# Performance work log

Hardware: AMD Instinct MI355X
Metric: run time of the kernel (lower is better)

Reference implementation:

```python
import jax, jax.numpy as jnp
import numpy as np

NUM_HEADS = 12
HEAD_SIZE = 64
HIDDEN = NUM_HEADS * HEAD_SIZE  # 768
SEQ = 4096


def setup_inputs() -> dict:
    key = jax.random.key(0)
    ks = jax.random.split(key, 7)
    s = 0.02
    return {
        "hidden_states": jax.random.normal(ks[0], (1, SEQ, HIDDEN), jnp.float32),
        "attention_mask": jnp.zeros((1, 1, 1, SEQ), jnp.float32),
        "Wq": jax.random.normal(ks[1], (HIDDEN, HIDDEN), jnp.float32) * s,
        "bq": jax.random.normal(ks[2], (HIDDEN,), jnp.float32) * s,
        "Wk": jax.random.normal(ks[3], (HIDDEN, HIDDEN), jnp.float32) * s,
        "bk": jax.random.normal(ks[4], (HIDDEN,), jnp.float32) * s,
        "Wv": jax.random.normal(ks[5], (HIDDEN, HIDDEN), jnp.float32) * s,
        "bv": jax.random.normal(ks[6], (HIDDEN,), jnp.float32) * s,
    }


def _split_heads(x):
    # [B, S, H] -> [B, nh, S, hd]
    B, S, _ = x.shape
    return x.reshape(B, S, NUM_HEADS, HEAD_SIZE).transpose(0, 2, 1, 3)


def reference(hidden_states, attention_mask, Wq, bq, Wk, bk, Wv, bv):
    # torch Linear: y = x @ W.T + b
    q = _split_heads(hidden_states @ Wq.T + bq)  # [B, nh, S, hd]
    k = _split_heads(hidden_states @ Wk.T + bk)
    scores = jnp.einsum("bhqd,bhkd->bhqk", q, k) / jnp.sqrt(
        jnp.asarray(HEAD_SIZE, hidden_states.dtype)
    )
    scores = scores + attention_mask  # broadcast [1,1,1,S]
    probs = jax.nn.softmax(scores, axis=-1)  # [B, nh, S, S]
    # multi_rand_attn_cuda is a Monte-Carlo approximation of the exact
    # aggregation: probs @ (hidden @ Wv.T + bv), per head. The reference
    # computes the exact expected value (deterministic equivalent).
    v = _split_heads(hidden_states @ Wv.T + bv)  # [B, nh, S, hd]
    ctx = jnp.einsum("bhqk,bhkd->bhqd", probs, v)  # [B, nh, S, hd]
    B, _, S, _ = ctx.shape
    ctx = ctx.transpose(0, 2, 1, 3).reshape(B, S, HIDDEN)
    return ctx
```

## Files before the change

kernel.cpp:

```cpp
#include <hip/hip_runtime.h>
#include <hip/hip_bf16.h>

#define SEQ 4096
#define HID 768
#define NHEAD 12
#define HDIM 64
#define KVB 64
#define NT (SEQ / KVB)
#define PBK 64
#define PNT (HID / PBK)

typedef __attribute__((ext_vector_type(8))) short bf16x8;
typedef __attribute__((ext_vector_type(4))) float f32x4;
typedef __attribute__((ext_vector_type(4))) short s16x4;

static __device__ __forceinline__ short f2bf(float f) {
    unsigned u = __builtin_bit_cast(unsigned, f);
    unsigned r = (u + 0x7fffu + ((u >> 16) & 1u)) >> 16;
    return (short)r;
}
static __device__ __forceinline__ unsigned cvtpk(float lo, float hi) {
    unsigned r;
    asm("v_cvt_pk_bf16_f32 %0, %1, %2" : "=v"(r) : "v"(lo), "v"(hi));
    return r;
}
static __device__ __forceinline__ float max3f(float a, float b, float c) {
    float r;
    asm("v_max3_f32 %0, %1, %2, %3" : "=v"(r) : "v"(a), "v"(b), "v"(c));
    return r;
}
static __device__ __forceinline__ void glds16(const void* g, void* l) {
    __builtin_amdgcn_global_load_lds(
        (const __attribute__((address_space(1))) unsigned*)g,
        (__attribute__((address_space(3))) unsigned*)l, 16, 0, 0);
}

__global__ __launch_bounds__(256) void cast_bf16_kernel(
    const float* __restrict__ src, short* __restrict__ dst)
{
    const size_t i = (size_t)blockIdx.x * 256 + threadIdx.x;
    const float4* s = reinterpret_cast<const float4*>(src) + i * 2;
    const float4 a = s[0], b = s[1];
    bf16x8 o;
    o[0] = f2bf(a.x); o[1] = f2bf(a.y); o[2] = f2bf(a.z); o[3] = f2bf(a.w);
    o[4] = f2bf(b.x); o[5] = f2bf(b.y); o[6] = f2bf(b.z); o[7] = f2bf(b.w);
    reinterpret_cast<bf16x8*>(dst)[i] = o;
}

__global__ __launch_bounds__(256) void cast_w_kernel(
    const float* __restrict__ Wq, const float* __restrict__ Wk,
    const float* __restrict__ Wv, short* __restrict__ dst)
{
    const int z = blockIdx.y;
    const float* src = (z == 0) ? Wq : ((z == 1) ? Wk : Wv);
    const size_t i = (size_t)blockIdx.x * 256 + threadIdx.x;
    const float4* s = reinterpret_cast<const float4*>(src) + i * 2;
    const float4 a = s[0], b = s[1];
    bf16x8 o;
    o[0] = f2bf(a.x); o[1] = f2bf(a.y); o[2] = f2bf(a.z); o[3] = f2bf(a.w);
    o[4] = f2bf(b.x); o[5] = f2bf(b.y); o[6] = f2bf(b.z); o[7] = f2bf(b.w);
    reinterpret_cast<bf16x8*>(dst + (size_t)z * HID * HID)[i] = o;
}

__global__ __launch_bounds__(256) void qkv_proj_kernel(
    const short* __restrict__ hsb, const short* __restrict__ Wb,
    const float* __restrict__ bq, const float* __restrict__ bk,
    const float* __restrict__ bv,
    short* __restrict__ Qb, short* __restrict__ Kb, short* __restrict__ Vt)
{
    __shared__ __align__(16) char lds[65536];
    const int z = blockIdx.z;
    const float* bias = (z == 0) ? bq : ((z == 1) ? bk : bv);

    const int lane = threadIdx.x & 63;
    const int w    = threadIdx.x >> 6;
    const int lr = lane & 15, hi = lane >> 4;
    const int wi = w >> 1, wj = w & 1;

    const short* Ag; const short* Bg; int ar0, br0;
    if (z < 2) { Ag = Wb + (size_t)z * HID * HID; ar0 = blockIdx.x * 128;
                 Bg = hsb;                        br0 = blockIdx.y * 128; }
    else       { Ag = hsb;                        ar0 = blockIdx.y * 128;
                 Bg = Wb + (size_t)2 * HID * HID; br0 = blockIdx.x * 128; }

    const int rsub = lane >> 3;
    const int c16  = (lane & 7) ^ rsub;

    auto stage = [&](int t, int buf) {
        const int k0 = t * PBK;
#pragma unroll
        for (int c = 0; c < 4; ++c) {
            const int ch = w * 4 + c;
            const int row = ch * 8 + rsub;
            glds16(Ag + (size_t)(ar0 + row) * HID + k0 + c16 * 8,
                   lds + buf * 16384 + ch * 1024);
            glds16(Bg + (size_t)(br0 + row) * HID + k0 + c16 * 8,
                   lds + 32768 + buf * 16384 + ch * 1024);
        }
    };

    stage(0, 0);
    f32x4 acc[4][4] = {};

    for (int t = 0; t < PNT; ++t) {
        asm volatile("s_waitcnt vmcnt(0)" ::: "memory");
        __builtin_amdgcn_s_barrier();
        __builtin_amdgcn_sched_barrier(0);
        if (t + 1 < PNT) stage(t + 1, (t + 1) & 1);
        const char* LA = lds + (t & 1) * 16384;
        const char* LB = lds + 32768 + (t & 1) * 16384;
#pragma unroll
        for (int ks = 0; ks < 2; ++ks) {
            bf16x8 af[4], bf_[4];
#pragma unroll
            for (int i = 0; i < 4; ++i) {
                const int rowA = wi * 64 + i * 16 + lr;
                af[i] = *reinterpret_cast<const bf16x8*>(
                    LA + rowA * 128 + (((ks * 4 + hi) ^ (rowA & 7)) << 4));
                const int rowB = wj * 64 + i * 16 + lr;
                bf_[i] = *reinterpret_cast<const bf16x8*>(
                    LB + rowB * 128 + (((ks * 4 + hi) ^ (rowB & 7)) << 4));
            }
            __builtin_amdgcn_s_setprio(1);
#pragma unroll
            for (int ia = 0; ia < 4; ++ia)
#pragma unroll
                for (int ib = 0; ib < 4; ++ib)
                    acc[ia][ib] = __builtin_amdgcn_mfma_f32_16x16x32_bf16(
                        af[ia], bf_[ib], acc[ia][ib], 0, 0, 0);
            __builtin_amdgcn_s_setprio(0);
        }
    }

    const float SCQ = 0.125f * 1.44269504088896340736f;
    if (z < 2) {
        short* outp = (z == 0) ? Qb : Kb;
        const float sc = (z == 0) ? SCQ : 1.0f;
#pragma unroll
        for (int ia = 0; ia < 4; ++ia) {
            const int nb = ar0 + wi * 64 + ia * 16 + hi * 4;
            const float4 b4 = *reinterpret_cast<const float4*>(bias + nb);
#pragma unroll
            for (int ib = 0; ib < 4; ++ib) {
                const int m = br0 + wj * 64 + ib * 16 + lr;
                s16x4 v;
                v[0] = f2bf((acc[ia][ib][0] + b4.x) * sc);
                v[1] = f2bf((acc[ia][ib][1] + b4.y) * sc);
                v[2] = f2bf((acc[ia][ib][2] + b4.z) * sc);
                v[3] = f2bf((acc[ia][ib][3] + b4.w) * sc);
                *reinterpret_cast<s16x4*>(outp + (size_t)m * HID + nb) = v;
            }
        }
    } else {
#pragma unroll
        for (int ib = 0; ib < 4; ++ib) {
            const int n = br0 + wj * 64 + ib * 16 + lr;
            const float bb = bias[n];
#pragma unroll
            for (int ia = 0; ia < 4; ++ia) {
                const int mb = ar0 + wi * 64 + ia * 16 + hi * 4;
                s16x4 v;
                v[0] = f2bf(acc[ia][ib][0] + bb);
                v[1] = f2bf(acc[ia][ib][1] + bb);
                v[2] = f2bf(acc[ia][ib][2] + bb);
                v[3] = f2bf(acc[ia][ib][3] + bb);
                *reinterpret_cast<s16x4*>(Vt + (size_t)n * SEQ + mb) = v;
            }
        }
    }
}

__global__ __launch_bounds__(512, 6) void attn_kernel(
    const short* __restrict__ Qb, const short* __restrict__ Kb,
    const short* __restrict__ Vt, const float* __restrict__ maskp,
    float* __restrict__ out)
{
    __shared__ __align__(16) char lds[49152];
    const int tid  = threadIdx.x;
    const int lane = tid & 63;
    const int w    = tid >> 6;
    const int lr = lane & 15, hi = lane >> 4;
    const int qh = w >> 1, kh = w & 1;
    const int head = blockIdx.y;
    const int q0 = blockIdx.x * 64 + qh * 16;
    const float ML = 1.44269504088896340736f;

    const int srow = lane >> 3;
    const int c16s = (lane & 7) ^ srow ^ ((w & 1) << 2);
    const int sofK = (w * 8 + srow) * HID + head * HDIM + c16s * 8;
    const int sofV = (head * HDIM + w * 8 + srow) * SEQ + c16s * 8;
    const short* gK = Kb;
    const short* gV = Vt;
    char* sdK = lds + w * 1024;
    char* sdV = lds + 16384 + w * 1024;

    auto stagep = [&](int buf) {
        glds16(gK + sofK, sdK + buf * 8192);
        glds16(gV + sofV, sdV + buf * 8192);
        gK += KVB * HID; gV += KVB;
    };

    stagep(0);

    {
        float* mb = (float*)(lds + 32768);
        const int base = tid * 8;
#pragma unroll
        for (int i = 0; i < 2; ++i) {
            float4 m4 = *reinterpret_cast<const float4*>(maskp + base + i * 4);
            m4.x *= ML; m4.y *= ML; m4.z *= ML; m4.w *= ML;
            *reinterpret_cast<float4*>(mb + base + i * 4) = m4;
        }
    }

    const short* qp = Qb + (size_t)(q0 + lr) * HID + head * HDIM + hi * 8;
    const bf16x8 qf0 = *reinterpret_cast<const bf16x8*>(qp);
    const bf16x8 qf1 = *reinterpret_cast<const bf16x8*>(qp + 32);

    __syncthreads();

    const int kbase = ((lr >> 2) * 8) + (lr & 3);
    const int krow0 = kh * 32 + kbase;
    const int fr0   = (krow0 & 7) ^ (((krow0 >> 3) & 1) << 2);
    const int o1    = (hi ^ fr0) << 4;
    const char* kpA = lds + krow0 * 128 + o1;
    const char* kpB = lds + krow0 * 128 + (o1 ^ 64);
    const int fv    = (lr & 7) ^ (((lr >> 3) & 1) << 2);
    const char* vpB = lds + 16384 + lr * 128 + (((kh * 4 + hi) ^ fv) << 4);
    const float* mptr = (const float*)(lds + 32768) + kh * 32 + hi * 8;

    f32x4 acc[4] = {};
    float m_r = -INFINITY, ls = 0.f;

    auto tile = [&](int tt, int buf) {
        asm volatile("s_waitcnt vmcnt(0)" ::: "memory");
        __builtin_amdgcn_s_barrier();
        __builtin_amdgcn_sched_barrier(0);
        if (tt + 1 < NT) stagep(buf ^ 1);

        const f32x4 ci0 = *reinterpret_cast<const f32x4*>(mptr);
        const f32x4 ci1 = *reinterpret_cast<const f32x4*>(mptr + 4);
        mptr += KVB;
        const int bo = buf * 8192;
        const bf16x8 kf00 = *reinterpret_cast<const bf16x8*>(kpA + bo);
        const bf16x8 kf01 = *reinterpret_cast<const bf16x8*>(kpB + bo);
        const bf16x8 kf10 = *reinterpret_cast<const bf16x8*>(kpB + bo + 512);
        const bf16x8 kf11 = *reinterpret_cast<const bf16x8*>(kpA + bo + 512);
        f32x4 z0 = ci0, z1 = ci1;
        __builtin_amdgcn_s_setprio(1);
        z0 = __builtin_amdgcn_mfma_f32_16x16x32_bf16(kf00, qf0, z0, 0, 0, 0);
        z0 = __builtin_amdgcn_mfma_f32_16x16x32_bf16(kf01, qf1, z0, 0, 0, 0);
        z1 = __builtin_amdgcn_mfma_f32_16x16x32_bf16(kf10, qf0, z1, 0, 0, 0);
        z1 = __builtin_amdgcn_mfma_f32_16x16x32_bf16(kf11, qf1, z1, 0, 0, 0);
        __builtin_amdgcn_s_setprio(0);

        float e0[4], e1[4];
#pragma unroll
        for (int r = 0; r < 4; ++r) {
            e0[r] = exp2f(z0[r] - m_r);
            e1[r] = exp2f(z1[r] - m_r);
        }

        const float pa = max3f(e0[0], e0[1], e0[2]);
        const float pb = max3f(e0[3], e1[0], e1[1]);
        const float pc = max3f(e1[2], e1[3], pa);
        const float pmax = fmaxf(pb, pc);
        if (__ballot(pmax > 256.f)) {
            float t_ = fmaxf(
                max3f(z0[0], z0[1], z0[2]),
                max3f(fmaxf(z0[3], z1[0]), fmaxf(z1[1], z1[2]), z1[3]));
            t_ = fmaxf(t_, __shfl_xor(t_, 16));
            t_ = fmaxf(t_, __shfl_xor(t_, 32));
            const float newm = fmaxf(m_r, t_);
            const float sc = exp2f(fmaxf(m_r - newm, -128.f));
            ls *= sc;
#pragma unroll
            for (int dg = 0; dg < 4; ++dg) acc[dg] *= sc;
            m_r = newm;
#pragma unroll
            for (int r = 0; r < 4; ++r) {
                e0[r] = exp2f(z0[r] - newm);
                e1[r] = exp2f(z1[r] - newm);
            }
        }

        ls += ((e0[0] + e0[1]) + (e0[2] + e0[3]))
            + ((e1[0] + e1[1]) + (e1[2] + e1[3]));
        union { unsigned u[4]; bf16x8 v; } P;
        P.u[0] = cvtpk(e0[0], e0[1]);
        P.u[1] = cvtpk(e0[2], e0[3]);
        P.u[2] = cvtpk(e1[0], e1[1]);
        P.u[3] = cvtpk(e1[2], e1[3]);

        __builtin_amdgcn_s_setprio(1);
#pragma unroll
        for (int dg = 0; dg < 4; ++dg) {
            const bf16x8 vf = *reinterpret_cast<const bf16x8*>(
                vpB + bo + dg * 2048);
            acc[dg] = __builtin_amdgcn_mfma_f32_16x16x32_bf16(vf, P.v, acc[dg], 0, 0, 0);
        }
        __builtin_amdgcn_s_setprio(0);
    };

#pragma unroll 1
    for (int t = 0; t < NT; t += 2) {
        tile(t, 0);
        tile(t + 1, 1);
    }

    ls += __shfl_xor(ls, 16);
    ls += __shfl_xor(ls, 32);

    __syncthreads();
    float* mg  = (float*)lds;
    float* mlb = (float*)(lds + 16384);
    if (kh == 1) {
        float2 v0; v0.x = m_r; v0.y = ls;
        *reinterpret_cast<float2*>(mlb + (qh * 64 + lane) * 2) = v0;
#pragma unroll
        for (int dg = 0; dg < 4; ++dg)
            *reinterpret_cast<f32x4*>(
                mg + ((qh * 4 + dg) * 64 + lane) * 4) = acc[dg];
    }
    __syncthreads();
    if (kh == 0) {
        const float2 v = *reinterpret_cast<const float2*>(
            mlb + (qh * 64 + lane) * 2);
        const float mm = fmaxf(m_r, v.x);
        const float sc0 = exp2f(fmaxf(m_r - mm, -128.f));
        const float sc1 = exp2f(fmaxf(v.x - mm, -128.f));
        const float rl = 1.0f / (ls * sc0 + v.y * sc1);
#pragma unroll
        for (int dg = 0; dg < 4; ++dg) {
            const f32x4 o1v = *reinterpret_cast<const f32x4*>(
                mg + ((qh * 4 + dg) * 64 + lane) * 4);
            const f32x4 of = (acc[dg] * sc0 + o1v * sc1) * rl;
            float* op = out + (size_t)(q0 + lr) * HID
                      + head * HDIM + dg * 16 + hi * 4;
            *reinterpret_cast<f32x4*>(op) = of;
        }
    }
}

extern "C" void kernel_launch(void* const* d_in, const int* in_sizes, int n_in,
                              void* d_out, int out_size, void* d_ws, size_t ws_size,
                              hipStream_t stream) {
    const float* hs   = (const float*)d_in[0];
    const float* mask = (const float*)d_in[1];
    const float* Wq   = (const float*)d_in[2];
    const float* bq   = (const float*)d_in[3];
    const float* Wk   = (const float*)d_in[4];
    const float* bk   = (const float*)d_in[5];
    const float* Wv   = (const float*)d_in[6];
    const float* bv   = (const float*)d_in[7];

    short* Qb = (short*)d_ws;
    short* Kb = Qb + (size_t)SEQ * HID;
    short* Vt = Kb + (size_t)SEQ * HID;
    float* out = (float*)d_out;

    short* hsb = (short*)d_out;
    short* Wb  = hsb + (size_t)SEQ * HID;

    cast_bf16_kernel<<<dim3(SEQ * HID / 2048), 256, 0, stream>>>(hs, hsb);
    cast_w_kernel<<<dim3(HID * HID / 2048, 3), 256, 0, stream>>>(Wq, Wk, Wv, Wb);

    qkv_proj_kernel<<<dim3(HID / 128, SEQ / 128, 3), 256, 0, stream>>>(
        hsb, Wb, bq, bk, bv, Qb, Kb, Vt);

    attn_kernel<<<dim3(SEQ / KVB, NHEAD), 512, 0, stream>>>(Qb, Kb, Vt, mask, out);
}
```

Before: 132.6 us.

## Double KV tile size to 128 per iteration in attention kernel

Each attention iteration now processes 128 keys instead of 64. Double-buffered K/V staging and LDS grow to 80 KB, and launch bounds drop to 4 blocks per CU. The larger tile halves the barrier and softmax-bookkeeping overhead per key and gives more MFMA work between syncs. In exchange it uses more registers and LDS, and occupancy falls from 6 to 4 blocks.

```diff
diff --git a/kernel.cpp b/kernel.cpp
--- a/kernel.cpp
+++ b/kernel.cpp
@@ -5,7 +5,7 @@
 #define HID 768
 #define NHEAD 12
 #define HDIM 64
-#define KVB 64
+#define KVB 128
 #define NT (SEQ / KVB)
 #define PBK 64
 #define PNT (HID / PBK)
@@ -170,12 +170,12 @@
     }
 }
 
-__global__ __launch_bounds__(512, 6) void attn_kernel(
+__global__ __launch_bounds__(512, 4) void attn_kernel(
     const short* __restrict__ Qb, const short* __restrict__ Kb,
     const short* __restrict__ Vt, const float* __restrict__ maskp,
     float* __restrict__ out)
 {
-    __shared__ __align__(16) char lds[49152];
+    __shared__ __align__(16) char lds[81920];
     const int tid  = threadIdx.x;
     const int lane = tid & 63;
     const int w    = tid >> 6;
@@ -186,24 +186,32 @@
     const float ML = 1.44269504088896340736f;
 
     const int srow = lane >> 3;
-    const int c16s = (lane & 7) ^ srow ^ ((w & 1) << 2);
-    const int sofK = (w * 8 + srow) * HID + head * HDIM + c16s * 8;
-    const int sofV = (head * HDIM + w * 8 + srow) * SEQ + c16s * 8;
+    const int c16k = (lane & 7) ^ srow ^ ((w & 1) << 2);
+    const int sofK0 = (w * 8 + srow) * HID + head * HDIM + c16k * 8;
+    const int sofK1 = sofK0 + 64 * HID;
+    const int sofV0 = (head * HDIM + (w & 7) * 8 + srow) * SEQ
+                    + (w >> 3) * 64 + c16k * 8;
+    const int sofV1 = sofV0 + 64;
     const short* gK = Kb;
     const short* gV = Vt;
-    char* sdK = lds + w * 1024;
-    char* sdV = lds + 16384 + w * 1024;
+    char* sdK0 = lds + w * 1024;
+    char* sdK1 = lds + (w + 8) * 1024;
+    char* sdV0 = lds + 32768 + w * 1024;
+    char* sdV1 = lds + 32768 + (w + 8) * 1024;
 
     auto stagep = [&](int buf) {
-        glds16(gK + sofK, sdK + buf * 8192);
-        glds16(gV + sofV, sdV + buf * 8192);
+        const int bo = buf * 16384;
+        glds16(gK + sofK0, sdK0 + bo);
+        glds16(gK + sofK1, sdK1 + bo);
+        glds16(gV + sofV0, sdV0 + bo);
+        glds16(gV + sofV1, sdV1 + bo);
         gK += KVB * HID; gV += KVB;
     };
 
     stagep(0);
 
     {
-        float* mb = (float*)(lds + 32768);
+        float* mb = (float*)(lds + 65536);
         const int base = tid * 8;
 #pragma unroll
         for (int i = 0; i < 2; ++i) {
@@ -220,14 +228,11 @@
     __syncthreads();
 
     const int kbase = ((lr >> 2) * 8) + (lr & 3);
-    const int krow0 = kh * 32 + kbase;
-    const int fr0   = (krow0 & 7) ^ (((krow0 >> 3) & 1) << 2);
-    const int o1    = (hi ^ fr0) << 4;
-    const char* kpA = lds + krow0 * 128 + o1;
-    const char* kpB = lds + krow0 * 128 + (o1 ^ 64);
+    const int fr0   = (kbase & 7) ^ (((kbase >> 3) & 1) << 2);
+    const char* kp0 = lds + (kh * 64 + kbase) * 128 + ((hi ^ fr0) << 4);
     const int fv    = (lr & 7) ^ (((lr >> 3) & 1) << 2);
-    const char* vpB = lds + 16384 + lr * 128 + (((kh * 4 + hi) ^ fv) << 4);
-    const float* mptr = (const float*)(lds + 32768) + kh * 32 + hi * 8;
+    const char* vp0 = lds + 32768 + kh * 8192 + lr * 128 + ((hi ^ fv) << 4);
+    const float* mptr = (const float*)(lds + 65536) + kh * 64 + hi * 8;
 
     f32x4 acc[4] = {};
     float m_r = -INFINITY, ls = 0.f;
@@ -240,35 +245,59 @@
 
         const f32x4 ci0 = *reinterpret_cast<const f32x4*>(mptr);
         const f32x4 ci1 = *reinterpret_cast<const f32x4*>(mptr + 4);
+        const f32x4 ci2 = *reinterpret_cast<const f32x4*>(mptr + 32);
+        const f32x4 ci3 = *reinterpret_cast<const f32x4*>(mptr + 36);
         mptr += KVB;
-        const int bo = buf * 8192;
-        const bf16x8 kf00 = *reinterpret_cast<const bf16x8*>(kpA + bo);
-        const bf16x8 kf01 = *reinterpret_cast<const bf16x8*>(kpB + bo);
-        const bf16x8 kf10 = *reinterpret_cast<const bf16x8*>(kpB + bo + 512);
-        const bf16x8 kf11 = *reinterpret_cast<const bf16x8*>(kpA + bo + 512);
-        f32x4 z0 = ci0, z1 = ci1;
+
+        const int bo = buf * 16384;
+        const char* kb = kp0 + bo;
+        const bf16x8 k00 = *reinterpret_cast<const bf16x8*>(kb);
+        const bf16x8 k01 = *reinterpret_cast<const bf16x8*>(
+            (const char*)((size_t)kb ^ 64));
+        const bf16x8 k10 = *reinterpret_cast<const bf16x8*>(
+            (const char*)((size_t)(kb + 512) ^ 64));
+        const bf16x8 k11 = *reinterpret_cast<const bf16x8*>(kb + 512);
+        const bf16x8 k20 = *reinterpret_cast<const bf16x8*>(kb + 4096);
+        const bf16x8 k21 = *reinterpret_cast<const bf16x8*>(
+            (const char*)((size_t)(kb + 4096) ^ 64));
+        const bf16x8 k30 = *reinterpret_cast<const bf16x8*>(
+            (const char*)((size_t)(kb + 4608) ^ 64));
+        const bf16x8 k31 = *reinterpret_cast<const bf16x8*>(kb + 4608);
+        f32x4 z0 = ci0, z1 = ci1, z2 = ci2, z3 = ci3;
         __builtin_amdgcn_s_setprio(1);
-        z0 = __builtin_amdgcn_mfma_f32_16x16x32_bf16(kf00, qf0, z0, 0, 0, 0);
-        z0 = __builtin_amdgcn_mfma_f32_16x16x32_bf16(kf01, qf1, z0, 0, 0, 0);
-        z1 = __builtin_amdgcn_mfma_f32_16x16x32_bf16(kf10, qf0, z1, 0, 0, 0);
-        z1 = __builtin_amdgcn_mfma_f32_16x16x32_bf16(kf11, qf1, z1, 0, 0, 0);
+        z0 = __builtin_amdgcn_mfma_f32_16x16x32_bf16(k00, qf0, z0, 0, 0, 0);
+        z0 = __builtin_amdgcn_mfma_f32_16x16x32_bf16(k01, qf1, z0, 0, 0, 0);
+        z1 = __builtin_amdgcn_mfma_f32_16x16x32_bf16(k10, qf0, z1, 0, 0, 0);
+        z1 = __builtin_amdgcn_mfma_f32_16x16x32_bf16(k11, qf1, z1, 0, 0, 0);
+        z2 = __builtin_amdgcn_mfma_f32_16x16x32_bf16(k20, qf0, z2, 0, 0, 0);
+        z2 = __builtin_amdgcn_mfma_f32_16x16x32_bf16(k21, qf1, z2, 0, 0, 0);
+        z3 = __builtin_amdgcn_mfma_f32_16x16x32_bf16(k30, qf0, z3, 0, 0, 0);
+        z3 = __builtin_amdgcn_mfma_f32_16x16x32_bf16(k31, qf1, z3, 0, 0, 0);
         __builtin_amdgcn_s_setprio(0);
 
-        float e0[4], e1[4];
+        float e0[4], e1[4], e2[4], e3[4];
 #pragma unroll
         for (int r = 0; r < 4; ++r) {
             e0[r] = exp2f(z0[r] - m_r);
             e1[r] = exp2f(z1[r] - m_r);
+            e2[r] = exp2f(z2[r] - m_r);
+            e3[r] = exp2f(z3[r] - m_r);
         }
 
         const float pa = max3f(e0[0], e0[1], e0[2]);
         const float pb = max3f(e0[3], e1[0], e1[1]);
-        const float pc = max3f(e1[2], e1[3], pa);
-        const float pmax = fmaxf(pb, pc);
+        const float pc = max3f(e1[2], e1[3], e2[0]);
+        const float pd = max3f(e2[1], e2[2], e2[3]);
+        const float pe = max3f(e3[0], e3[1], e3[2]);
+        const float pmax = max3f(fmaxf(pa, pb), fmaxf(pc, pd),
+                                 fmaxf(pe, e3[3]));
         if (__ballot(pmax > 256.f)) {
             float t_ = fmaxf(
-                max3f(z0[0], z0[1], z0[2]),
-                max3f(fmaxf(z0[3], z1[0]), fmaxf(z1[1], z1[2]), z1[3]));
+                fmaxf(max3f(z0[0], z0[1], z0[2]),
+                      max3f(z0[3], z1[0], z1[1])),
+                fmaxf(max3f(z1[2], z1[3], z2[0]),
+                      fmaxf(max3f(z2[1], z2[2], z2[3]),
+                            fmaxf(max3f(z3[0], z3[1], z3[2]), z3[3]))));
             t_ = fmaxf(t_, __shfl_xor(t_, 16));
             t_ = fmaxf(t_, __shfl_xor(t_, 32));
             const float newm = fmaxf(m_r, t_);
@@ -281,23 +310,30 @@
             for (int r = 0; r < 4; ++r) {
                 e0[r] = exp2f(z0[r] - newm);
                 e1[r] = exp2f(z1[r] - newm);
+                e2[r] = exp2f(z2[r] - newm);
+                e3[r] = exp2f(z3[r] - newm);
             }
         }
 
-        ls += ((e0[0] + e0[1]) + (e0[2] + e0[3]))
-            + ((e1[0] + e1[1]) + (e1[2] + e1[3]));
-        union { unsigned u[4]; bf16x8 v; } P;
-        P.u[0] = cvtpk(e0[0], e0[1]);
-        P.u[1] = cvtpk(e0[2], e0[3]);
-        P.u[2] = cvtpk(e1[0], e1[1]);
-        P.u[3] = cvtpk(e1[2], e1[3]);
-
+        ls += (((e0[0] + e0[1]) + (e0[2] + e0[3]))
+             + ((e1[0] + e1[1]) + (e1[2] + e1[3])))
+            + (((e2[0] + e2[1]) + (e2[2] + e2[3]))
+             + ((e3[0] + e3[1]) + (e3[2] + e3[3])));
+        union { unsigned u[4]; bf16x8 v; } P0, P1;
+        P0.u[0] = cvtpk(e0[0], e0[1]); P0.u[1] = cvtpk(e0[2], e0[3]);
+        P0.u[2] = cvtpk(e1[0], e1[1]); P0.u[3] = cvtpk(e1[2], e1[3]);
+        P1.u[0] = cvtpk(e2[0], e2[1]); P1.u[1] = cvtpk(e2[2], e2[3]);
+        P1.u[2] = cvtpk(e3[0], e3[1]); P1.u[3] = cvtpk(e3[2], e3[3]);
+
+        const char* vb = vp0 + bo;
         __builtin_amdgcn_s_setprio(1);
 #pragma unroll
         for (int dg = 0; dg < 4; ++dg) {
-            const bf16x8 vf = *reinterpret_cast<const bf16x8*>(
-                vpB + bo + dg * 2048);
-            acc[dg] = __builtin_amdgcn_mfma_f32_16x16x32_bf16(vf, P.v, acc[dg], 0, 0, 0);
+            const bf16x8 vf0 = *reinterpret_cast<const bf16x8*>(vb + dg * 2048);
+            const bf16x8 vf1 = *reinterpret_cast<const bf16x8*>(
+                (const char*)((size_t)(vb + dg * 2048) ^ 64));
+            acc[dg] = __builtin_amdgcn_mfma_f32_16x16x32_bf16(vf0, P0.v, acc[dg], 0, 0, 0);
+            acc[dg] = __builtin_amdgcn_mfma_f32_16x16x32_bf16(vf1, P1.v, acc[dg], 0, 0, 0);
         }
         __builtin_amdgcn_s_setprio(0);
     };
@@ -368,5 +404,5 @@
     qkv_proj_kernel<<<dim3(HID / 128, SEQ / 128, 3), 256, 0, stream>>>(
         hsb, Wb, bq, bk, bv, Qb, Kb, Vt);
 
-    attn_kernel<<<dim3(SEQ / KVB, NHEAD), 512, 0, stream>>>(Qb, Kb, Vt, mask, out);
-}
+    attn_kernel<<<dim3(SEQ / 64, NHEAD), 512, 0, stream>>>(Qb, Kb, Vt, mask, out);
+}
```

New measurement: 166.0 us. +25.1%, slower.

## Software-pipeline PV MFMA one tile behind and merge cast kernels

Applied to the files above, without the earlier changes.

The attention loop now issues the previous tile's P·V MFMAs right after the current tile's QK MFMAs, so matrix work overlaps with the exp/softmax ALU work of the current tile. V gets a triple-buffered LDS ring (with a zeroed dummy buffer for the first step), which raises LDS use to 64KB and lowers the occupancy hint from 6 to 4. Separately, the two fp32→bf16 cast kernels are merged into one launch to save a kernel launch. The trade-off is lower occupancy and more registers held for the deferred P fragment.

```diff
diff --git a/kernel.cpp b/kernel.cpp
--- a/kernel.cpp
+++ b/kernel.cpp
@@ -35,31 +35,28 @@
         (__attribute__((address_space(3))) unsigned*)l, 16, 0, 0);
 }
 
-__global__ __launch_bounds__(256) void cast_bf16_kernel(
-    const float* __restrict__ src, short* __restrict__ dst)
+__global__ __launch_bounds__(256) void cast_all_kernel(
+    const float* __restrict__ hs, const float* __restrict__ Wq,
+    const float* __restrict__ Wk, const float* __restrict__ Wv,
+    short* __restrict__ hsb, short* __restrict__ Wb)
 {
     const size_t i = (size_t)blockIdx.x * 256 + threadIdx.x;
-    const float4* s = reinterpret_cast<const float4*>(src) + i * 2;
-    const float4 a = s[0], b = s[1];
+    const float* s; short* d; size_t idx;
+    if (i < 393216) {
+        s = hs; d = hsb; idx = i;
+    } else {
+        size_t j = i - 393216;
+        int z = (int)(j / 73728);
+        idx = j - (size_t)z * 73728;
+        s = (z == 0) ? Wq : ((z == 1) ? Wk : Wv);
+        d = Wb + (size_t)z * HID * HID;
+    }
+    const float4* sp = reinterpret_cast<const float4*>(s) + idx * 2;
+    const float4 a = sp[0], b = sp[1];
     bf16x8 o;
     o[0] = f2bf(a.x); o[1] = f2bf(a.y); o[2] = f2bf(a.z); o[3] = f2bf(a.w);
     o[4] = f2bf(b.x); o[5] = f2bf(b.y); o[6] = f2bf(b.z); o[7] = f2bf(b.w);
-    reinterpret_cast<bf16x8*>(dst)[i] = o;
-}
-
-__global__ __launch_bounds__(256) void cast_w_kernel(
-    const float* __restrict__ Wq, const float* __restrict__ Wk,
-    const float* __restrict__ Wv, short* __restrict__ dst)
-{
-    const int z = blockIdx.y;
-    const float* src = (z == 0) ? Wq : ((z == 1) ? Wk : Wv);
-    const size_t i = (size_t)blockIdx.x * 256 + threadIdx.x;
-    const float4* s = reinterpret_cast<const float4*>(src) + i * 2;
-    const float4 a = s[0], b = s[1];
-    bf16x8 o;
-    o[0] = f2bf(a.x); o[1] = f2bf(a.y); o[2] = f2bf(a.z); o[3] = f2bf(a.w);
-    o[4] = f2bf(b.x); o[5] = f2bf(b.y); o[6] = f2bf(b.z); o[7] = f2bf(b.w);
-    reinterpret_cast<bf16x8*>(dst + (size_t)z * HID * HID)[i] = o;
+    reinterpret_cast<bf16x8*>(d)[idx] = o;
 }
 
 __global__ __launch_bounds__(256) void qkv_proj_kernel(
@@ -170,12 +167,12 @@
     }
 }
 
-__global__ __launch_bounds__(512, 6) void attn_kernel(
+__global__ __launch_bounds__(512, 4) void attn_kernel(
     const short* __restrict__ Qb, const short* __restrict__ Kb,
     const short* __restrict__ Vt, const float* __restrict__ maskp,
     float* __restrict__ out)
 {
-    __shared__ __align__(16) char lds[49152];
+    __shared__ __align__(16) char lds[65536];
     const int tid  = threadIdx.x;
     const int lane = tid & 63;
     const int w    = tid >> 6;
@@ -194,16 +191,16 @@
     char* sdK = lds + w * 1024;
     char* sdV = lds + 16384 + w * 1024;
 
-    auto stagep = [&](int buf) {
-        glds16(gK + sofK, sdK + buf * 8192);
-        glds16(gV + sofV, sdV + buf * 8192);
+    auto stagep = [&](int kb, int vb) {
+        glds16(gK + sofK, sdK + kb * 8192);
+        glds16(gV + sofV, sdV + vb * 8192);
         gK += KVB * HID; gV += KVB;
     };
 
-    stagep(0);
+    stagep(0, 0);
 
     {
-        float* mb = (float*)(lds + 32768);
+        float* mb = (float*)(lds + 49152);
         const int base = tid * 8;
 #pragma unroll
         for (int i = 0; i < 2; ++i) {
@@ -211,6 +208,11 @@
             m4.x *= ML; m4.y *= ML; m4.z *= ML; m4.w *= ML;
             *reinterpret_cast<float4*>(mb + base + i * 4) = m4;
         }
+    }
+
+    {
+        f32x4 zz = {};
+        *reinterpret_cast<f32x4*>(lds + 16384 + 3 * 8192 + w * 1024 + lane * 16) = zz;
     }
 
     const short* qp = Qb + (size_t)(q0 + lr) * HID + head * HDIM + hi * 8;
@@ -227,31 +229,39 @@
     const char* kpB = lds + krow0 * 128 + (o1 ^ 64);
     const int fv    = (lr & 7) ^ (((lr >> 3) & 1) << 2);
     const char* vpB = lds + 16384 + lr * 128 + (((kh * 4 + hi) ^ fv) << 4);
-    const float* mptr = (const float*)(lds + 32768) + kh * 32 + hi * 8;
+    const float* mptr = (const float*)(lds + 49152) + kh * 32 + hi * 8;
 
     f32x4 acc[4] = {};
     float m_r = -INFINITY, ls = 0.f;
-
-    auto tile = [&](int tt, int buf) {
+    union { unsigned u[4]; bf16x8 v; } Pp;
+    Pp.u[0] = 0; Pp.u[1] = 0; Pp.u[2] = 0; Pp.u[3] = 0;
+
+    auto tile = [&](int tt, int kb, int vbn, int vbp) {
         asm volatile("s_waitcnt vmcnt(0)" ::: "memory");
         __builtin_amdgcn_s_barrier();
         __builtin_amdgcn_sched_barrier(0);
-        if (tt + 1 < NT) stagep(buf ^ 1);
+        if (tt + 1 < NT) stagep(kb ^ 1, vbn);
 
         const f32x4 ci0 = *reinterpret_cast<const f32x4*>(mptr);
         const f32x4 ci1 = *reinterpret_cast<const f32x4*>(mptr + 4);
         mptr += KVB;
-        const int bo = buf * 8192;
+        const int bo = kb * 8192;
         const bf16x8 kf00 = *reinterpret_cast<const bf16x8*>(kpA + bo);
         const bf16x8 kf01 = *reinterpret_cast<const bf16x8*>(kpB + bo);
         const bf16x8 kf10 = *reinterpret_cast<const bf16x8*>(kpB + bo + 512);
         const bf16x8 kf11 = *reinterpret_cast<const bf16x8*>(kpA + bo + 512);
         f32x4 z0 = ci0, z1 = ci1;
+        const char* vb = vpB + vbp * 8192;
         __builtin_amdgcn_s_setprio(1);
         z0 = __builtin_amdgcn_mfma_f32_16x16x32_bf16(kf00, qf0, z0, 0, 0, 0);
         z0 = __builtin_amdgcn_mfma_f32_16x16x32_bf16(kf01, qf1, z0, 0, 0, 0);
         z1 = __builtin_amdgcn_mfma_f32_16x16x32_bf16(kf10, qf0, z1, 0, 0, 0);
         z1 = __builtin_amdgcn_mfma_f32_16x16x32_bf16(kf11, qf1, z1, 0, 0, 0);
+#pragma unroll
+        for (int dg = 0; dg < 4; ++dg) {
+            const bf16x8 vf = *reinterpret_cast<const bf16x8*>(vb + dg * 2048);
+            acc[dg] = __builtin_amdgcn_mfma_f32_16x16x32_bf16(vf, Pp.v, acc[dg], 0, 0, 0);
+        }
         __builtin_amdgcn_s_setprio(0);
 
         float e0[4], e1[4];
@@ -286,26 +296,29 @@
 
         ls += ((e0[0] + e0[1]) + (e0[2] + e0[3]))
             + ((e1[0] + e1[1]) + (e1[2] + e1[3]));
-        union { unsigned u[4]; bf16x8 v; } P;
-        P.u[0] = cvtpk(e0[0], e0[1]);
-        P.u[1] = cvtpk(e0[2], e0[3]);
-        P.u[2] = cvtpk(e1[0], e1[1]);
-        P.u[3] = cvtpk(e1[2], e1[3]);
-
+        Pp.u[0] = cvtpk(e0[0], e0[1]);
+        Pp.u[1] = cvtpk(e0[2], e0[3]);
+        Pp.u[2] = cvtpk(e1[0], e1[1]);
+        Pp.u[3] = cvtpk(e1[2], e1[3]);
+    };
+
+#pragma unroll 1
+    for (int t = 0; t < NT; t += 4) {
+        tile(t,     0, 1, 3);
+        tile(t + 1, 1, 2, 0);
+        tile(t + 2, 0, 3, 1);
+        tile(t + 3, 1, 0, 2);
+    }
+
+    {
+        const char* vb = vpB + 3 * 8192;
         __builtin_amdgcn_s_setprio(1);
 #pragma unroll
         for (int dg = 0; dg < 4; ++dg) {
-            const bf16x8 vf = *reinterpret_cast<const bf16x8*>(
-                vpB + bo + dg * 2048);
-            acc[dg] = __builtin_amdgcn_mfma_f32_16x16x32_bf16(vf, P.v, acc[dg], 0, 0, 0);
+            const bf16x8 vf = *reinterpret_cast<const bf16x8*>(vb + dg * 2048);
+            acc[dg] = __builtin_amdgcn_mfma_f32_16x16x32_bf16(vf, Pp.v, acc[dg], 0, 0, 0);
         }
         __builtin_amdgcn_s_setprio(0);
-    };
-
-#pragma unroll 1
-    for (int t = 0; t < NT; t += 2) {
-        tile(t, 0);
-        tile(t + 1, 1);
     }
 
     ls += __shfl_xor(ls, 16);
@@ -362,8 +375,7 @@
     short* hsb = (short*)d_out;
     short* Wb  = hsb + (size_t)SEQ * HID;
 
-    cast_bf16_kernel<<<dim3(SEQ * HID / 2048), 256, 0, stream>>>(hs, hsb);
-    cast_w_kernel<<<dim3(HID * HID / 2048, 3), 256, 0, stream>>>(Wq, Wk, Wv, Wb);
+    cast_all_kernel<<<dim3(2400), 256, 0, stream>>>(hs, Wq, Wk, Wv, hsb, Wb);
 
     qkv_proj_kernel<<<dim3(HID / 128, SEQ / 128, 3), 256, 0, stream>>>(
         hsb, Wb, bq, bk, bv, Qb, Kb, Vt);
```

New measurement: 135.4 us. 2.0% more time.

## Merge cast kernels, precompute scaled mask globally, shrink attention LDS

Applied to the files above, without the earlier changes.

Folds the hidden-state cast, weight cast and mask pre-scaling into one launch, dropping a kernel launch. The attention kernel now reads the log2e-scaled mask from global memory instead of staging it in LDS, which cuts LDS to 32 KB and removes the occupancy hint from launch bounds. Mask loads are placed before the next tile's async K/V staging, with scheduling barriers around them. The trade is extra global or cache traffic for the mask in every tile and an added workspace buffer.

```diff
diff --git a/kernel.cpp b/kernel.cpp
--- a/kernel.cpp
+++ b/kernel.cpp
@@ -35,31 +35,41 @@
         (__attribute__((address_space(3))) unsigned*)l, 16, 0, 0);
 }
 
-__global__ __launch_bounds__(256) void cast_bf16_kernel(
-    const float* __restrict__ src, short* __restrict__ dst)
+__global__ __launch_bounds__(256) void cast_all_kernel(
+    const float* __restrict__ hs, const float* __restrict__ Wq,
+    const float* __restrict__ Wk, const float* __restrict__ Wv,
+    const float* __restrict__ mask,
+    short* __restrict__ hsb, short* __restrict__ Wb,
+    float* __restrict__ maskML)
 {
+    const float ML = 1.44269504088896340736f;
     const size_t i = (size_t)blockIdx.x * 256 + threadIdx.x;
-    const float4* s = reinterpret_cast<const float4*>(src) + i * 2;
-    const float4 a = s[0], b = s[1];
+    if (i >= 614400) {
+        const size_t j = i - 614400;
+        const float4* sp = reinterpret_cast<const float4*>(mask) + j * 2;
+        float4 a = sp[0], b = sp[1];
+        a.x *= ML; a.y *= ML; a.z *= ML; a.w *= ML;
+        b.x *= ML; b.y *= ML; b.z *= ML; b.w *= ML;
+        float4* dp = reinterpret_cast<float4*>(maskML) + j * 2;
+        dp[0] = a; dp[1] = b;
+        return;
+    }
+    const float* s; short* d; size_t idx;
+    if (i < 393216) {
+        s = hs; d = hsb; idx = i;
+    } else {
+        size_t j = i - 393216;
+        int z = (int)(j / 73728);
+        idx = j - (size_t)z * 73728;
+        s = (z == 0) ? Wq : ((z == 1) ? Wk : Wv);
+        d = Wb + (size_t)z * HID * HID;
+    }
+    const float4* sp = reinterpret_cast<const float4*>(s) + idx * 2;
+    const float4 a = sp[0], b = sp[1];
     bf16x8 o;
     o[0] = f2bf(a.x); o[1] = f2bf(a.y); o[2] = f2bf(a.z); o[3] = f2bf(a.w);
     o[4] = f2bf(b.x); o[5] = f2bf(b.y); o[6] = f2bf(b.z); o[7] = f2bf(b.w);
-    reinterpret_cast<bf16x8*>(dst)[i] = o;
-}
-
-__global__ __launch_bounds__(256) void cast_w_kernel(
-    const float* __restrict__ Wq, const float* __restrict__ Wk,
-    const float* __restrict__ Wv, short* __restrict__ dst)
-{
-    const int z = blockIdx.y;
-    const float* src = (z == 0) ? Wq : ((z == 1) ? Wk : Wv);
-    const size_t i = (size_t)blockIdx.x * 256 + threadIdx.x;
-    const float4* s = reinterpret_cast<const float4*>(src) + i * 2;
-    const float4 a = s[0], b = s[1];
-    bf16x8 o;
-    o[0] = f2bf(a.x); o[1] = f2bf(a.y); o[2] = f2bf(a.z); o[3] = f2bf(a.w);
-    o[4] = f2bf(b.x); o[5] = f2bf(b.y); o[6] = f2bf(b.z); o[7] = f2bf(b.w);
-    reinterpret_cast<bf16x8*>(dst + (size_t)z * HID * HID)[i] = o;
+    reinterpret_cast<bf16x8*>(d)[idx] = o;
 }
 
 __global__ __launch_bounds__(256) void qkv_proj_kernel(
@@ -170,12 +180,12 @@
     }
 }
 
-__global__ __launch_bounds__(512, 6) void attn_kernel(
+__global__ __launch_bounds__(512) void attn_kernel(
     const short* __restrict__ Qb, const short* __restrict__ Kb,
-    const short* __restrict__ Vt, const float* __restrict__ maskp,
+    const short* __restrict__ Vt, const float* __restrict__ maskml,
     float* __restrict__ out)
 {
-    __shared__ __align__(16) char lds[49152];
+    __shared__ __align__(16) char lds[32768];
     const int tid  = threadIdx.x;
     const int lane = tid & 63;
     const int w    = tid >> 6;
@@ -183,7 +193,6 @@
     const int qh = w >> 1, kh = w & 1;
     const int head = blockIdx.y;
     const int q0 = blockIdx.x * 64 + qh * 16;
-    const float ML = 1.44269504088896340736f;
 
     const int srow = lane >> 3;
     const int c16s = (lane & 7) ^ srow ^ ((w & 1) << 2);
@@ -202,17 +211,6 @@
 
     stagep(0);
 
-    {
-        float* mb = (float*)(lds + 32768);
-        const int base = tid * 8;
-#pragma unroll
-        for (int i = 0; i < 2; ++i) {
-            float4 m4 = *reinterpret_cast<const float4*>(maskp + base + i * 4);
-            m4.x *= ML; m4.y *= ML; m4.z *= ML; m4.w *= ML;
-            *reinterpret_cast<float4*>(mb + base + i * 4) = m4;
-        }
-    }
-
     const short* qp = Qb + (size_t)(q0 + lr) * HID + head * HDIM + hi * 8;
     const bf16x8 qf0 = *reinterpret_cast<const bf16x8*>(qp);
     const bf16x8 qf1 = *reinterpret_cast<const bf16x8*>(qp + 32);
@@ -227,7 +225,7 @@
     const char* kpB = lds + krow0 * 128 + (o1 ^ 64);
     const int fv    = (lr & 7) ^ (((lr >> 3) & 1) << 2);
     const char* vpB = lds + 16384 + lr * 128 + (((kh * 4 + hi) ^ fv) << 4);
-    const float* mptr = (const float*)(lds + 32768) + kh * 32 + hi * 8;
+    const float* mptr = maskml + kh * 32 + hi * 8;
 
     f32x4 acc[4] = {};
     float m_r = -INFINITY, ls = 0.f;
@@ -236,11 +234,13 @@
         asm volatile("s_waitcnt vmcnt(0)" ::: "memory");
         __builtin_amdgcn_s_barrier();
         __builtin_amdgcn_sched_barrier(0);
-        if (tt + 1 < NT) stagep(buf ^ 1);
-
         const f32x4 ci0 = *reinterpret_cast<const f32x4*>(mptr);
         const f32x4 ci1 = *reinterpret_cast<const f32x4*>(mptr + 4);
         mptr += KVB;
+        __builtin_amdgcn_sched_barrier(0);
+        if (tt + 1 < NT) stagep(buf ^ 1);
+        __builtin_amdgcn_sched_barrier(0);
+
         const int bo = buf * 8192;
         const bf16x8 kf00 = *reinterpret_cast<const bf16x8*>(kpA + bo);
         const bf16x8 kf01 = *reinterpret_cast<const bf16x8*>(kpB + bo);
@@ -357,16 +357,17 @@
     short* Qb = (short*)d_ws;
     short* Kb = Qb + (size_t)SEQ * HID;
     short* Vt = Kb + (size_t)SEQ * HID;
+    float* maskML = (float*)(Vt + (size_t)HID * SEQ);
     float* out = (float*)d_out;
 
     short* hsb = (short*)d_out;
     short* Wb  = hsb + (size_t)SEQ * HID;
 
-    cast_bf16_kernel<<<dim3(SEQ * HID / 2048), 256, 0, stream>>>(hs, hsb);
-    cast_w_kernel<<<dim3(HID * HID / 2048, 3), 256, 0, stream>>>(Wq, Wk, Wv, Wb);
+    cast_all_kernel<<<dim3(2402), 256, 0, stream>>>(
+        hs, Wq, Wk, Wv, mask, hsb, Wb, maskML);
 
     qkv_proj_kernel<<<dim3(HID / 128, SEQ / 128, 3), 256, 0, stream>>>(
         hsb, Wb, bq, bk, bv, Qb, Kb, Vt);
 
-    attn_kernel<<<dim3(SEQ / KVB, NHEAD), 512, 0, stream>>>(Qb, Kb, Vt, mask, out);
-}
+    attn_kernel<<<dim3(SEQ / KVB, NHEAD), 512, 0, stream>>>(Qb, Kb, Vt, maskML, out);
+}
```

Result: slower. 135.8 us (+2.4%).
